# Performance work log

Hardware: AMD Instinct MI355X
Metric: run time of the kernel (lower is better)

Reference implementation:

```python
import jax, jax.numpy as jnp
import numpy as np

NBASE = 4                       # number of bases (DNA)
NSTATE = 2 * NBASE * (NBASE + 1)  # = 40 flip-flop transition states
SCALE = 5.0
LARGE_LOG_VAL = 50000.0


def setup_inputs() -> dict:
    key = jax.random.key(0)
    kx, kw, kb = jax.random.split(key, 3)
    T, N, INSIZE = 2048, 128, 256
    x = jax.random.normal(kx, (T, N, INSIZE), dtype=jnp.float32)
    # orthonormal-ish init approximated by scaled gaussian
    W = jax.random.normal(kw, (NSTATE, INSIZE), dtype=jnp.float32) / np.float32(np.sqrt(INSIZE))
    b = 0.5 * jax.random.normal(kb, (NSTATE,), dtype=jnp.float32)
    return {"x": x, "W": W, "b": b}


def _log_partition_flipflop(scores):
    """Forward-algorithm log partition function. scores: (T, N, C)."""
    T, N, C = scores.shape
    fwd0 = jnp.concatenate(
        [jnp.zeros((N, NBASE), scores.dtype),
         jnp.full((N, NBASE), -LARGE_LOG_VAL, scores.dtype)], axis=1)
    logZ0 = jax.nn.logsumexp(fwd0, axis=1, keepdims=True)  # (N, 1)
    fwd0 = fwd0 - logZ0

    def step(carry, scores_t):
        fwd, logZ = carry
        # (N, nbase+1, 2*nbase): to-state grouped transition scores
        curr = fwd[:, None, :] + scores_t.reshape(N, NBASE + 1, 2 * NBASE)
        base1 = jax.nn.logsumexp(curr[:, :NBASE], axis=2)            # (N, nbase) flip states
        base2 = jnp.logaddexp(curr[:, NBASE, :NBASE],
                              curr[:, NBASE, NBASE:])               # (N, nbase) flop states
        new_state = jnp.concatenate([base1, base2], axis=1)          # (N, 2*nbase)
        factors = jax.nn.logsumexp(new_state, axis=1, keepdims=True)  # (N, 1)
        return (new_state - factors, logZ + factors), None

    (_, logZ), _ = jax.lax.scan(step, (fwd0, logZ0), scores)
    return logZ  # (N, 1)


def reference(x, W, b):
    T = x.shape[0]
    # scale * tanh(x W^T + b) -> transition scores (T, N, NSTATE)
    y = SCALE * jnp.tanh(jnp.einsum('tni,ci->tnc', x, W) + b)
    logZ = _log_partition_flipflop(y)          # (N, 1)
    return y - logZ / np.float32(T)            # broadcast over T and C
```

## Files before the change

kernel.cpp:

```cpp
#include <hip/hip_runtime.h>
#include <hip/hip_bf16.h>

#define T_DIM 2048
#define N_DIM 128
#define K_DIM 256
#define C_DIM 40
#define SEG 256
#define SEGLEN 8
#define GRP 8
#define SEGPERGRP 32

typedef __attribute__((ext_vector_type(8))) short bf16x8;
typedef __attribute__((ext_vector_type(4))) float f32x4v;

__device__ __forceinline__ unsigned pack_bf16(float a, float b) {
    union { float f; unsigned u; } ua, ub;
    ua.f = a; ub.f = b;
    unsigned ra = (ua.u + 0x7FFFu + ((ua.u >> 16) & 1u)) >> 16;
    unsigned rb = (ub.u + 0x7FFFu + ((ub.u >> 16) & 1u)) >> 16;
    return (ra & 0xFFFFu) | (rb << 16);
}

__device__ __forceinline__ float fast_tanh(float v) {
    float e = __expf(2.f * v);
    return 1.f - 2.f / (e + 1.f);
}

__global__ __launch_bounds__(256, 2) void k_gemm_tanh(
    const float* __restrict__ x, const float* __restrict__ W,
    const float* __restrict__ b, float* __restrict__ y)
{
    __shared__ __align__(16) float shX[4][2][16][128];

    const int tid = threadIdx.x;
    const int lane = tid & 63;
    const int wave = tid >> 6;
    const int lr = lane & 15;
    const int kg = lane >> 4;
    const int gw = blockIdx.x * 4 + wave;
    const int t0 = gw * 8;
    const int aswz = (lr & 7) << 4;

    bf16x8 wf[3][8];
    #pragma unroll
    for (int cb = 0; cb < 3; ++cb) {
        #pragma unroll
        for (int kk = 0; kk < 8; ++kk) {
            int rowc = cb * 16 + lr;
            float4 w0 = {0.f, 0.f, 0.f, 0.f}, w1 = {0.f, 0.f, 0.f, 0.f};
            if (rowc < C_DIM) {
                const float* wp = W + rowc * K_DIM + kg * 8 + kk * 32;
                w0 = *reinterpret_cast<const float4*>(wp);
                w1 = *reinterpret_cast<const float4*>(wp + 4);
            }
            union { bf16x8 v; unsigned u[4]; } uw;
            uw.u[0] = pack_bf16(w0.x, w0.y);
            uw.u[1] = pack_bf16(w0.z, w0.w);
            uw.u[2] = pack_bf16(w1.x, w1.y);
            uw.u[3] = pack_bf16(w1.z, w1.w);
            wf[cb][kk] = uw.v;
        }
    }

    float4 bia0 = *reinterpret_cast<const float4*>(b + kg * 4);
    float4 bia1 = *reinterpret_cast<const float4*>(b + 16 + kg * 4);
    float4 bia2 = {0.f, 0.f, 0.f, 0.f};
    if (kg < 2) bia2 = *reinterpret_cast<const float4*>(b + 32 + kg * 4);

    auto stage = [&](int h) {
        int tile = t0 + (h >> 1);
        const char* gbase = reinterpret_cast<const char*>(x)
                          + (size_t)tile * 16384 + (h & 1) * 512;
        float* lbase = &shX[wave][h & 1][0][0];
        #pragma unroll
        for (int j = 0; j < 8; ++j) {
            int r = 2 * j + (lane >> 5);
            int off = ((lane & 31) * 16) ^ ((r & 7) << 4);
            const void* gp = gbase + r * 1024 + off;
            __builtin_amdgcn_global_load_lds(
                (const __attribute__((address_space(1))) void*)gp,
                (__attribute__((address_space(3))) void*)(lbase + j * 256),
                16, 0, 0);
        }
    };

    f32x4v acc0, acc1, acc2;

#define COMPUTE_HALF(KH)                                                          \
    do {                                                                          \
        const char* cX = reinterpret_cast<const char*>(&shX[wave][KH][0][0]);     \
        _Pragma("unroll")                                                         \
        for (int kt = 0; kt < 4; ++kt) {                                          \
            int k0 = kg * 32 + kt * 128;                                          \
            float4 d0 = *reinterpret_cast<const float4*>(cX + lr * 512 + (k0 ^ aswz));        \
            float4 d1 = *reinterpret_cast<const float4*>(cX + lr * 512 + ((k0 + 16) ^ aswz)); \
            union { bf16x8 v; unsigned u[4]; } xf;                                \
            xf.u[0] = pack_bf16(d0.x, d0.y);                                      \
            xf.u[1] = pack_bf16(d0.z, d0.w);                                      \
            xf.u[2] = pack_bf16(d1.x, d1.y);                                      \
            xf.u[3] = pack_bf16(d1.z, d1.w);                                      \
            acc0 = __builtin_amdgcn_mfma_f32_16x16x32_bf16(wf[0][KH * 4 + kt], xf.v, acc0, 0, 0, 0); \
            acc1 = __builtin_amdgcn_mfma_f32_16x16x32_bf16(wf[1][KH * 4 + kt], xf.v, acc1, 0, 0, 0); \
            acc2 = __builtin_amdgcn_mfma_f32_16x16x32_bf16(wf[2][KH * 4 + kt], xf.v, acc2, 0, 0, 0); \
        }                                                                         \
    } while (0)

    stage(0);
    stage(1);

    for (int t = 0; t < 8; ++t) {
        __builtin_amdgcn_sched_barrier(0);
        asm volatile("s_waitcnt vmcnt(8)" ::: "memory");
        __builtin_amdgcn_sched_barrier(0);
        acc0 = (f32x4v){0.f, 0.f, 0.f, 0.f};
        acc1 = (f32x4v){0.f, 0.f, 0.f, 0.f};
        acc2 = (f32x4v){0.f, 0.f, 0.f, 0.f};
        COMPUTE_HALF(0);
        __builtin_amdgcn_sched_barrier(0);
        if (t < 7) stage(2 * t + 2);

        __builtin_amdgcn_sched_barrier(0);
        if (t < 7) asm volatile("s_waitcnt vmcnt(8)" ::: "memory");
        else       asm volatile("s_waitcnt vmcnt(0)" ::: "memory");
        __builtin_amdgcn_sched_barrier(0);
        COMPUTE_HALF(1);

        size_t row = (size_t)(t0 + t) * 16 + lr;
        float* yr = y + row * C_DIM;
        float4 o0, o1;
        o0.x = 5.f * fast_tanh(acc0[0] + bia0.x);
        o0.y = 5.f * fast_tanh(acc0[1] + bia0.y);
        o0.z = 5.f * fast_tanh(acc0[2] + bia0.z);
        o0.w = 5.f * fast_tanh(acc0[3] + bia0.w);
        o1.x = 5.f * fast_tanh(acc1[0] + bia1.x);
        o1.y = 5.f * fast_tanh(acc1[1] + bia1.y);
        o1.z = 5.f * fast_tanh(acc1[2] + bia1.z);
        o1.w = 5.f * fast_tanh(acc1[3] + bia1.w);
        *reinterpret_cast<float4*>(yr + kg * 4) = o0;
        *reinterpret_cast<float4*>(yr + 16 + kg * 4) = o1;
        if (kg < 2) {
            float4 o2;
            o2.x = 5.f * fast_tanh(acc2[0] + bia2.x);
            o2.y = 5.f * fast_tanh(acc2[1] + bia2.y);
            o2.z = 5.f * fast_tanh(acc2[2] + bia2.z);
            o2.w = 5.f * fast_tanh(acc2[3] + bia2.w);
            *reinterpret_cast<float4*>(yr + 32 + kg * 4) = o2;
        }

        __builtin_amdgcn_sched_barrier(0);
        if (t < 7) stage(2 * t + 3);
    }
#undef COMPUTE_HALF
}

__global__ __launch_bounds__(128) void k_seg(
    const float* __restrict__ y, float* __restrict__ segv, float* __restrict__ segl)
{
    int tid = blockIdx.x * 128 + threadIdx.x;
    int n = tid & 127;
    int s = tid >> 7;

    float P[8][8];
    #pragma unroll
    for (int j = 0; j < 8; ++j)
        #pragma unroll
        for (int c = 0; c < 8; ++c) P[j][c] = (j == c) ? 1.f : 0.f;

    for (int st = 0; st < SEGLEN; ++st) {
        int t = s * SEGLEN + st;
        const float* yr = y + ((size_t)t * N_DIM + n) * C_DIM;
        float e[40];
        #pragma unroll
        for (int i = 0; i < 10; ++i) {
            float4 v = reinterpret_cast<const float4*>(yr)[i];
            e[i * 4 + 0] = __expf(v.x);
            e[i * 4 + 1] = __expf(v.y);
            e[i * 4 + 2] = __expf(v.z);
            e[i * 4 + 3] = __expf(v.w);
        }
        #pragma unroll
        for (int c = 0; c < 8; ++c) {
            float np[8];
            #pragma unroll
            for (int j = 0; j < 4; ++j) {
                float a = 0.f;
                #pragma unroll
                for (int i = 0; i < 8; ++i) a += P[i][c] * e[j * 8 + i];
                np[j] = a;
            }
            #pragma unroll
            for (int j = 0; j < 4; ++j)
                np[4 + j] = P[j][c] * e[32 + j] + P[4 + j][c] * e[36 + j];
            #pragma unroll
            for (int j = 0; j < 8; ++j) P[j][c] = np[j];
        }
    }
    #pragma unroll
    for (int c = 0; c < 8; ++c) {
        float sum = 0.f;
        #pragma unroll
        for (int j = 0; j < 8; ++j) sum += P[j][c];
        float inv = 1.f / sum;
        #pragma unroll
        for (int j = 0; j < 8; ++j)
            segv[(((size_t)s * 8 + c) * 8 + j) * N_DIM + n] = P[j][c] * inv;
        segl[((size_t)s * 8 + c) * N_DIM + n] = __logf(sum);
    }
}

__global__ __launch_bounds__(256) void k_grp(
    const float* __restrict__ segv, const float* __restrict__ segl,
    float* __restrict__ grpv, float* __restrict__ grpl)
{
    int tid = blockIdx.x * 256 + threadIdx.x;
    int n = tid & 127;
    int cc = (tid >> 7) & 7;
    int g = tid >> 10;

    float u[8];
    #pragma unroll
    for (int i = 0; i < 8; ++i) u[i] = (i == cc) ? 1.f : 0.f;
    float logacc = 0.f;

    for (int s = g * SEGPERGRP; s < (g + 1) * SEGPERGRP; ++s) {
        float l[8];
        #pragma unroll
        for (int i = 0; i < 8; ++i) l[i] = segl[((size_t)s * 8 + i) * N_DIM + n];
        float m = l[0];
        #pragma unroll
        for (int i = 1; i < 8; ++i) m = fmaxf(m, l[i]);
        float nu[8] = {0.f, 0.f, 0.f, 0.f, 0.f, 0.f, 0.f, 0.f};
        #pragma unroll
        for (int i = 0; i < 8; ++i) {
            float wi = u[i] * __expf(l[i] - m);
            #pragma unroll
            for (int j = 0; j < 8; ++j)
                nu[j] += wi * segv[(((size_t)s * 8 + i) * 8 + j) * N_DIM + n];
        }
        float sum = 0.f;
        #pragma unroll
        for (int j = 0; j < 8; ++j) sum += nu[j];
        float inv = 1.f / sum;
        #pragma unroll
        for (int j = 0; j < 8; ++j) u[j] = nu[j] * inv;
        logacc += m + __logf(sum);
    }
    #pragma unroll
    for (int j = 0; j < 8; ++j)
        grpv[(((size_t)g * 8 + cc) * 8 + j) * N_DIM + n] = u[j];
    grpl[((size_t)g * 8 + cc) * N_DIM + n] = logacc;
}

__global__ void k_fin(const float* __restrict__ grpv, const float* __restrict__ grpl,
                      float* __restrict__ lz)
{
    int n = threadIdx.x;
    float p[8] = {0.25f, 0.25f, 0.25f, 0.25f, 0.f, 0.f, 0.f, 0.f};
    float logZ = 1.3862943611198906f;

    for (int g = 0; g < GRP; ++g) {
        float l[8];
        #pragma unroll
        for (int i = 0; i < 8; ++i) l[i] = grpl[((size_t)g * 8 + i) * N_DIM + n];
        float m = l[0];
        #pragma unroll
        for (int i = 1; i < 8; ++i) m = fmaxf(m, l[i]);
        float nu[8] = {0.f, 0.f, 0.f, 0.f, 0.f, 0.f, 0.f, 0.f};
        #pragma unroll
        for (int i = 0; i < 8; ++i) {
            float wi = p[i] * __expf(l[i] - m);
            #pragma unroll
            for (int j = 0; j < 8; ++j)
                nu[j] += wi * grpv[(((size_t)g * 8 + i) * 8 + j) * N_DIM + n];
        }
        float sum = 0.f;
        #pragma unroll
        for (int j = 0; j < 8; ++j) sum += nu[j];
        float inv = 1.f / sum;
        #pragma unroll
        for (int j = 0; j < 8; ++j) p[j] = nu[j] * inv;
        logZ += m + __logf(sum);
    }
    lz[n] = logZ * (1.f / (float)T_DIM);
}

__global__ __launch_bounds__(256) void k_sub(float* __restrict__ out,
                                             const float* __restrict__ lz)
{
    int i = blockIdx.x * 256 + threadIdx.x;
    int n = (i / 10) & 127;
    float d = lz[n];
    float4* o = reinterpret_cast<float4*>(out) + i;
    float4 v = *o;
    v.x -= d; v.y -= d; v.z -= d; v.w -= d;
    *o = v;
}

extern "C" void kernel_launch(void* const* d_in, const int* in_sizes, int n_in,
                              void* d_out, int out_size, void* d_ws, size_t ws_size,
                              hipStream_t stream) {
    const float* x = (const float*)d_in[0];
    const float* W = (const float*)d_in[1];
    const float* b = (const float*)d_in[2];
    float* out = (float*)d_out;
    float* ws = (float*)d_ws;

    float* segv = ws;
    float* segl = ws + 2097152;
    float* grpv = ws + 2359296;
    float* grpl = ws + 2424832;
    float* lz   = ws + 2433024;

    k_gemm_tanh<<<512, 256, 0, stream>>>(x, W, b, out);
    k_seg<<<256, 128, 0, stream>>>(out, segv, segl);
    k_grp<<<32, 256, 0, stream>>>(segv, segl, grpv, grpl);
    k_fin<<<1, 128, 0, stream>>>(grpv, grpl, lz);
    k_sub<<<10240, 256, 0, stream>>>(out, lz);
}
```

Before: 148.5 us.

## Stage GEMM input through registers and stride tiles across waves

Replaces the direct global-to-LDS async loads, which used double-buffered LDS and manual vmcnt waits, with register-staged float4 loads that are then written into a single LDS buffer per wave. Register prefetch of the next half-tile provides the overlap. Tile assignment also changes from contiguous 8 tiles per wave to a stride of 2048 tiles, so that concurrently running waves touch adjacent memory. This halves LDS use and may raise occupancy, but it costs registers and ds_write instructions. It also drops the hand-placed scheduling barriers, leaving the overlap to the compiler.

Measured after the change: 176.9 us. 1.19x slower.

```diff
diff --git a/kernel.cpp b/kernel.cpp
--- a/kernel.cpp
+++ b/kernel.cpp
@@ -30,7 +30,7 @@
     const float* __restrict__ x, const float* __restrict__ W,
     const float* __restrict__ b, float* __restrict__ y)
 {
-    __shared__ __align__(16) float shX[4][2][16][128];
+    __shared__ __align__(16) float shX[4][16][128];
 
     const int tid = threadIdx.x;
     const int lane = tid & 63;
@@ -38,8 +38,9 @@
     const int lr = lane & 15;
     const int kg = lane >> 4;
     const int gw = blockIdx.x * 4 + wave;
-    const int t0 = gw * 8;
     const int aswz = (lr & 7) << 4;
+    const int lhalf = lane >> 5;
+    const int loff = (lane & 31) * 16;
 
     bf16x8 wf[3][8];
     #pragma unroll
@@ -67,65 +68,63 @@
     float4 bia2 = {0.f, 0.f, 0.f, 0.f};
     if (kg < 2) bia2 = *reinterpret_cast<const float4*>(b + 32 + kg * 4);
 
-    auto stage = [&](int h) {
-        int tile = t0 + (h >> 1);
-        const char* gbase = reinterpret_cast<const char*>(x)
-                          + (size_t)tile * 16384 + (h & 1) * 512;
-        float* lbase = &shX[wave][h & 1][0][0];
-        #pragma unroll
-        for (int j = 0; j < 8; ++j) {
-            int r = 2 * j + (lane >> 5);
-            int off = ((lane & 31) * 16) ^ ((r & 7) << 4);
-            const void* gp = gbase + r * 1024 + off;
-            __builtin_amdgcn_global_load_lds(
-                (const __attribute__((address_space(1))) void*)gp,
-                (__attribute__((address_space(3))) void*)(lbase + j * 256),
-                16, 0, 0);
-        }
-    };
-
-    f32x4v acc0, acc1, acc2;
-
-#define COMPUTE_HALF(KH)                                                          \
-    do {                                                                          \
-        const char* cX = reinterpret_cast<const char*>(&shX[wave][KH][0][0]);     \
-        _Pragma("unroll")                                                         \
-        for (int kt = 0; kt < 4; ++kt) {                                          \
-            int k0 = kg * 32 + kt * 128;                                          \
-            float4 d0 = *reinterpret_cast<const float4*>(cX + lr * 512 + (k0 ^ aswz));        \
-            float4 d1 = *reinterpret_cast<const float4*>(cX + lr * 512 + ((k0 + 16) ^ aswz)); \
-            union { bf16x8 v; unsigned u[4]; } xf;                                \
-            xf.u[0] = pack_bf16(d0.x, d0.y);                                      \
-            xf.u[1] = pack_bf16(d0.z, d0.w);                                      \
-            xf.u[2] = pack_bf16(d1.x, d1.y);                                      \
-            xf.u[3] = pack_bf16(d1.z, d1.w);                                      \
-            acc0 = __builtin_amdgcn_mfma_f32_16x16x32_bf16(wf[0][KH * 4 + kt], xf.v, acc0, 0, 0, 0); \
-            acc1 = __builtin_amdgcn_mfma_f32_16x16x32_bf16(wf[1][KH * 4 + kt], xf.v, acc1, 0, 0, 0); \
-            acc2 = __builtin_amdgcn_mfma_f32_16x16x32_bf16(wf[2][KH * 4 + kt], xf.v, acc2, 0, 0, 0); \
-        }                                                                         \
+    const char* xb = reinterpret_cast<const char*>(x);
+    char* lds = reinterpret_cast<char*>(&shX[wave][0][0]);
+
+    float4 rA[8], rB[8];
+
+#define LOAD8(R, t, kh)                                                        \
+    do {                                                                       \
+        const char* base_ = xb + ((size_t)(t) * 2048 + gw) * 16384 + (kh) * 512; \
+        _Pragma("unroll")                                                      \
+        for (int j = 0; j < 8; ++j)                                            \
+            R[j] = *reinterpret_cast<const float4*>(base_ + (2 * j + lhalf) * 1024 + loff); \
     } while (0)
 
-    stage(0);
-    stage(1);
+#define WRITE8(R)                                                              \
+    do {                                                                       \
+        _Pragma("unroll")                                                      \
+        for (int j = 0; j < 8; ++j) {                                          \
+            int row_ = 2 * j + lhalf;                                          \
+            int adr_ = row_ * 512 + (loff ^ ((row_ & 7) << 4));                \
+            *reinterpret_cast<float4*>(lds + adr_) = R[j];                     \
+        }                                                                      \
+    } while (0)
+
+#define COMPUTE_HALF(KH)                                                       \
+    do {                                                                       \
+        _Pragma("unroll")                                                      \
+        for (int kt = 0; kt < 4; ++kt) {                                       \
+            int k0 = kg * 32 + kt * 128;                                       \
+            float4 d0 = *reinterpret_cast<const float4*>(lds + lr * 512 + (k0 ^ aswz));        \
+            float4 d1 = *reinterpret_cast<const float4*>(lds + lr * 512 + ((k0 + 16) ^ aswz)); \
+            union { bf16x8 v; unsigned u[4]; } xf;                             \
+            xf.u[0] = pack_bf16(d0.x, d0.y);                                   \
+            xf.u[1] = pack_bf16(d0.z, d0.w);                                   \
+            xf.u[2] = pack_bf16(d1.x, d1.y);                                   \
+            xf.u[3] = pack_bf16(d1.z, d1.w);                                   \
+            acc0 = __builtin_amdgcn_mfma_f32_16x16x32_bf16(wf[0][(KH) * 4 + kt], xf.v, acc0, 0, 0, 0); \
+            acc1 = __builtin_amdgcn_mfma_f32_16x16x32_bf16(wf[1][(KH) * 4 + kt], xf.v, acc1, 0, 0, 0); \
+            acc2 = __builtin_amdgcn_mfma_f32_16x16x32_bf16(wf[2][(KH) * 4 + kt], xf.v, acc2, 0, 0, 0); \
+        }                                                                      \
+    } while (0)
+
+    LOAD8(rA, 0, 0);
 
     for (int t = 0; t < 8; ++t) {
-        __builtin_amdgcn_sched_barrier(0);
-        asm volatile("s_waitcnt vmcnt(8)" ::: "memory");
-        __builtin_amdgcn_sched_barrier(0);
-        acc0 = (f32x4v){0.f, 0.f, 0.f, 0.f};
-        acc1 = (f32x4v){0.f, 0.f, 0.f, 0.f};
-        acc2 = (f32x4v){0.f, 0.f, 0.f, 0.f};
+        f32x4v acc0 = {0.f, 0.f, 0.f, 0.f};
+        f32x4v acc1 = {0.f, 0.f, 0.f, 0.f};
+        f32x4v acc2 = {0.f, 0.f, 0.f, 0.f};
+
+        LOAD8(rB, t, 1);
+        WRITE8(rA);
         COMPUTE_HALF(0);
-        __builtin_amdgcn_sched_barrier(0);
-        if (t < 7) stage(2 * t + 2);
-
-        __builtin_amdgcn_sched_barrier(0);
-        if (t < 7) asm volatile("s_waitcnt vmcnt(8)" ::: "memory");
-        else       asm volatile("s_waitcnt vmcnt(0)" ::: "memory");
-        __builtin_amdgcn_sched_barrier(0);
+
+        if (t < 7) LOAD8(rA, t + 1, 0);
+        WRITE8(rB);
         COMPUTE_HALF(1);
 
-        size_t row = (size_t)(t0 + t) * 16 + lr;
+        size_t row = ((size_t)t * 2048 + gw) * 16 + lr;
         float* yr = y + row * C_DIM;
         float4 o0, o1;
         o0.x = 5.f * fast_tanh(acc0[0] + bia0.x);
@@ -146,10 +145,9 @@
             o2.w = 5.f * fast_tanh(acc2[3] + bia2.w);
             *reinterpret_cast<float4*>(yr + 32 + kg * 4) = o2;
         }
-
-        __builtin_amdgcn_sched_barrier(0);
-        if (t < 7) stage(2 * t + 3);
-    }
+    }
+#undef LOAD8
+#undef WRITE8
 #undef COMPUTE_HALF
 }
 
```
